# Performance work log

Measured on AMD Instinct MI355X. Metric: run time of the kernel, lower is better.

## Reference

```python
import jax, jax.numpy as jnp
import numpy as np

NEG_INF = -1e20

def setup_inputs() -> dict:
    key = jax.random.key(0)
    kq, kk, kv, km = jax.random.split(key, 4)
    B, S, H, D = 2, 2048, 16, 64
    queries = jax.random.normal(kq, (B, S, H, D), dtype=jnp.float32)
    keys = jax.random.normal(kk, (B, S, H, D), dtype=jnp.float32)
    values = jax.random.normal(kv, (B, S, H, D), dtype=jnp.float32)
    mask = jax.random.randint(km, (B, 1, 1, S), 0, 2, dtype=jnp.int32)
    return {"queries": queries, "keys": keys, "values": values, "mask": mask}

def reference(queries, keys, values, mask):
    # scores: [B, H, Q, K]
    dk = keys.shape[-1]
    scores = jnp.einsum('bqhd,bkhd->bhqk', queries, keys) / jnp.sqrt(jnp.asarray(dk, queries.dtype))
    scores = jnp.where(mask == 0, jnp.asarray(NEG_INF, scores.dtype), scores)
    attn = jax.nn.softmax(scores, axis=-1)
    # dropout p=0.0 (eval): identity
    out = jnp.einsum('bhqv,bvhd->bqhd', attn, values)
    return out
```

## Files before the change

### kernel.cpp

```cpp
#include <hip/hip_runtime.h>
#include <hip/hip_bf16.h>

#define S_LEN 2048
#define NH 16
#define HD 64

typedef __attribute__((ext_vector_type(8))) __bf16 bf16x8;
typedef __attribute__((ext_vector_type(16))) float f32x16;

#define QSCALE 0.1803368801111204f

static __device__ __forceinline__ ushort f2bf(float f) {
    unsigned int u = __float_as_uint(f);
    u += 0x7fffu + ((u >> 16) & 1u);
    return (ushort)(u >> 16);
}

static __device__ __forceinline__ void gload16(const void* g, void* l) {
    __builtin_amdgcn_global_load_lds(
        (const __attribute__((address_space(1))) unsigned int*)g,
        (__attribute__((address_space(3))) unsigned int*)l, 16, 0, 0);
}
static __device__ __forceinline__ void gload4(const void* g, void* l) {
    __builtin_amdgcn_global_load_lds(
        (const __attribute__((address_space(1))) unsigned int*)g,
        (__attribute__((address_space(3))) unsigned int*)l, 4, 0, 0);
}

static __device__ __forceinline__ unsigned cvtpk_bf16(float lo, float hi) {
    unsigned r;
    asm("v_cvt_pk_bf16_f32 %0, %1, %2" : "=v"(r) : "v"(lo), "v"(hi));
    return r;
}
static __device__ __forceinline__ float exp2_fast(float x) {
    float r;
    asm("v_exp_f32 %0, %1" : "=v"(r) : "v"(x));
    return r;
}

__global__ __launch_bounds__(256) void prep_k_kernel(const float* __restrict__ in,
                                                     ushort* __restrict__ out) {
    unsigned t = blockIdx.x * 256u + threadIdx.x;
    unsigned o = t & 7u;
    unsigned s = (t >> 3) & 2047u;
    unsigned bh = t >> 14;
    unsigned b = bh >> 4, h = bh & 15u;
    const float* src = in + (((size_t)(b * S_LEN) + s) * NH + h) * HD + o * 8;
    float4 x = *(const float4*)src;
    float4 y = *(const float4*)(src + 4);
    union { ushort u[8]; uint4 q; } fu;
    fu.u[0] = f2bf(x.x); fu.u[1] = f2bf(x.y); fu.u[2] = f2bf(x.z); fu.u[3] = f2bf(x.w);
    fu.u[4] = f2bf(y.x); fu.u[5] = f2bf(y.y); fu.u[6] = f2bf(y.z); fu.u[7] = f2bf(y.w);
    unsigned kt = s >> 6, kh = (s >> 5) & 1u, kl = s & 31u;
    unsigned dchunk = o >> 1, ho = o & 1u;
    size_t ci = (((size_t)(bh * 32u + kt) * 2u + kh) * 4u + dchunk) * 64u + kl + 32u * ho;
    *(uint4*)(out + ci * 8u) = fu.q;
}

__global__ __launch_bounds__(256) void prep_v_kernel(const float* __restrict__ in,
                                                     ushort* __restrict__ out) {
    __shared__ float T[64][68];
    const unsigned tid = threadIdx.x;
    const unsigned kt = blockIdx.x, bh = blockIdx.y;
    const unsigned b = bh >> 4, h = bh & 15u;
#pragma unroll
    for (int i = 0; i < 4; ++i) {
        unsigned idx = tid + i * 256u;
        unsigned sl = idx >> 4, d4 = (idx & 15u) * 4u;
        float4 v = *(const float4*)(in + (((size_t)(b * S_LEN) + kt * 64u + sl) * NH + h) * HD + d4);
        *(float4*)&T[sl][d4] = v;
    }
    __syncthreads();
#pragma unroll
    for (int it = 0; it < 2; ++it) {
        unsigned ct = tid + it * 256u;
        unsigned l = ct & 63u, sub = ct >> 6;
        unsigned nt = sub & 1u, c = (sub >> 1) & 1u, kh = sub >> 2;
        unsigned d = (l & 31u) + 32u * nt;
        unsigned kb = kh * 32u + c * 16u + (l >> 5) * 8u;
        union { ushort u[8]; uint4 q; } fu;
#pragma unroll
        for (int j = 0; j < 8; ++j) fu.u[j] = f2bf(T[kb + j][d]);
        *(uint4*)(out + ((size_t)(bh * 32u + kt) * 8u + sub) * 512u + l * 8u) = fu.q;
    }
}

struct TileMem {
    ushort K[2][3][2048];
    ushort V[2][3][2048];
    int    mk[2][1024];
};
struct CombMem {
    float ob[4][32][64];
    float lsb[4][64];
    float rls[4][32];
};
union SMemU { TileMem s; CombMem c; };

__global__ __launch_bounds__(512, 4) void attn_kernel(const float* __restrict__ Qp,
                                                      const ushort* __restrict__ Kws,
                                                      const ushort* __restrict__ Vws,
                                                      const int* __restrict__ maskp,
                                                      float* __restrict__ outp) {
    __shared__ __align__(16) SMemU sm;

    const unsigned tid = threadIdx.x;
    const unsigned wid = tid >> 6;
    const unsigned lane = tid & 63u;
    const unsigned l31 = lane & 31u;
    const unsigned hi = lane >> 5;
    const unsigned qsub = wid & 3u;
    const unsigned kgrp = wid >> 2;

    const unsigned bh = blockIdx.y;
    const unsigned b = bh >> 4, h = bh & 15u;
    const unsigned q0 = blockIdx.x * 128u + qsub * 32u;

    bf16x8 qf[4];
    {
        const float* qb = Qp + (((size_t)(b * S_LEN) + q0 + l31) * NH + h) * HD + hi * 8u;
#pragma unroll
        for (int dc = 0; dc < 4; ++dc) {
            float4 x = *(const float4*)(qb + dc * 16);
            float4 y = *(const float4*)(qb + dc * 16 + 4);
            union { ushort u[8]; bf16x8 v; } fu;
            fu.u[0] = f2bf(x.x * QSCALE); fu.u[1] = f2bf(x.y * QSCALE);
            fu.u[2] = f2bf(x.z * QSCALE); fu.u[3] = f2bf(x.w * QSCALE);
            fu.u[4] = f2bf(y.x * QSCALE); fu.u[5] = f2bf(y.y * QSCALE);
            fu.u[6] = f2bf(y.z * QSCALE); fu.u[7] = f2bf(y.w * QSCALE);
            qf[dc] = fu.v;
        }
    }

    f32x16 oacc0 = {0,0,0,0,0,0,0,0,0,0,0,0,0,0,0,0};
    f32x16 oacc1 = {0,0,0,0,0,0,0,0,0,0,0,0,0,0,0,0};
    float ls0 = 0.f, ls1 = 0.f, ls2 = 0.f, ls3 = 0.f;

    const char* kgp = (const char*)(Kws + (size_t)bh * 131072u
                    + (size_t)kgrp * 65536u) + qsub * 1024u + lane * 16u;
    const char* vgp = (const char*)(Vws + (size_t)bh * 131072u
                    + (size_t)kgrp * 65536u) + qsub * 1024u + lane * 16u;

    ushort* klb = &sm.s.K[kgrp][0][qsub * 512u];
    ushort* vlb = &sm.s.V[kgrp][0][qsub * 512u];
    const ushort* krd = &sm.s.K[kgrp][0][0];
    const ushort* vrd = &sm.s.V[kgrp][0][0];

#define STAGE(T, BUF) do {                                                     \
    const size_t toff = (size_t)(T) * 4096u;                                   \
    gload16(kgp + toff, klb + (BUF) * 2048u);                                  \
    gload16(vgp + toff, vlb + (BUF) * 2048u);                                  \
  } while (0)

    {
        const int* mgp = maskp + (size_t)b * S_LEN + kgrp * 1024u + qsub * 256u + lane;
#pragma unroll
        for (int j = 0; j < 4; ++j)
            gload4(mgp + j * 64, &sm.s.mk[kgrp][qsub * 256u + j * 64u]);
    }
    STAGE(0, 0u);
    STAGE(1, 1u);
    asm volatile("s_waitcnt vmcnt(2)" ::: "memory");
    __builtin_amdgcn_s_barrier();

    unsigned cur = 0u, st = 2u;
    for (int t = 0; t < 32; ++t) {
        if (t < 30) STAGE(t + 2, st);
        const ushort* kr = krd + cur * 2048u;
        const ushort* vr = vrd + cur * 2048u;
        const int*    mr = &sm.s.mk[kgrp][(unsigned)t * 32u];

        bf16x8 kf[4];
#pragma unroll
        for (int dc = 0; dc < 4; ++dc)
            kf[dc] = *(const bf16x8*)&kr[dc * 512u + lane * 8u];

        f32x16 s = {0,0,0,0,0,0,0,0,0,0,0,0,0,0,0,0};
        __builtin_amdgcn_s_setprio(1);
#pragma unroll
        for (int dc = 0; dc < 4; ++dc)
            s = __builtin_amdgcn_mfma_f32_32x32x16_bf16(kf[dc], qf[dc], s, 0, 0, 0);
        __builtin_amdgcn_s_setprio(0);

        float p[16];
#pragma unroll
        for (int r1 = 0; r1 < 4; ++r1) {
            int mv[4];
            *(int4*)mv = *(const int4*)&mr[r1 * 8 + hi * 4];
#pragma unroll
            for (int r0 = 0; r0 < 4; ++r0) {
                const int reg = r1 * 4 + r0;
                p[reg] = exp2_fast(mv[r0] ? s[reg] : -1e30f);
            }
            ls0 += p[r1 * 4 + 0]; ls1 += p[r1 * 4 + 1];
            ls2 += p[r1 * 4 + 2]; ls3 += p[r1 * 4 + 3];
        }

#pragma unroll
        for (int c = 0; c < 2; ++c) {
            unsigned a0 = cvtpk_bf16(p[8 * c + 0], p[8 * c + 1]);
            unsigned a1 = cvtpk_bf16(p[8 * c + 2], p[8 * c + 3]);
            unsigned b0 = cvtpk_bf16(p[8 * c + 4], p[8 * c + 5]);
            unsigned b1 = cvtpk_bf16(p[8 * c + 6], p[8 * c + 7]);
            asm("v_permlane32_swap_b32 %0, %1" : "+v"(a0), "+v"(b0));
            asm("v_permlane32_swap_b32 %0, %1" : "+v"(a1), "+v"(b1));
            union { unsigned w[4]; bf16x8 v; } pa;
            pa.w[0] = a0; pa.w[1] = a1; pa.w[2] = b0; pa.w[3] = b1;
            bf16x8 vf0 = *(const bf16x8*)&vr[(c * 2 + 0) * 512u + lane * 8u];
            bf16x8 vf1 = *(const bf16x8*)&vr[(c * 2 + 1) * 512u + lane * 8u];
            __builtin_amdgcn_s_setprio(1);
            oacc0 = __builtin_amdgcn_mfma_f32_32x32x16_bf16(pa.v, vf0, oacc0, 0, 0, 0);
            oacc1 = __builtin_amdgcn_mfma_f32_32x32x16_bf16(pa.v, vf1, oacc1, 0, 0, 0);
            __builtin_amdgcn_s_setprio(0);
        }

        if (t < 30) asm volatile("s_waitcnt vmcnt(2)" ::: "memory");
        else        asm volatile("s_waitcnt vmcnt(0)" ::: "memory");
        __builtin_amdgcn_s_barrier();
        cur = (cur == 2u) ? 0u : cur + 1u;
        st  = (st  == 2u) ? 0u : st  + 1u;
    }
#undef STAGE

    float lsum = (ls0 + ls1) + (ls2 + ls3);
    lsum += __shfl_xor(lsum, 32);

    if (kgrp == 1) {
#pragma unroll
        for (int r = 0; r < 16; ++r) {
            sm.c.ob[qsub][r][lane]      = oacc0[r];
            sm.c.ob[qsub][16 + r][lane] = oacc1[r];
        }
        sm.c.lsb[qsub][lane] = lsum;
    }
    __syncthreads();
    if (kgrp == 0) {
        lsum += sm.c.lsb[qsub][lane];
#pragma unroll
        for (int r = 0; r < 16; ++r) {
            oacc0[r] += sm.c.ob[qsub][r][lane];
            oacc1[r] += sm.c.ob[qsub][16 + r][lane];
        }
        if (hi == 0) sm.c.rls[qsub][l31] = 1.0f / lsum;
#pragma unroll
        for (int r1 = 0; r1 < 4; ++r1) {
#pragma unroll
            for (int r0 = 0; r0 < 4; ++r0) {
                const int reg = r1 * 4 + r0;
                const unsigned q = r0 + 8u * r1 + 4u * hi;
                const float rr = sm.c.rls[qsub][q];
                float* ob = outp + (((size_t)(b * S_LEN) + q0 + q) * NH + h) * HD + l31;
                ob[0]  = oacc0[reg] * rr;
                ob[32] = oacc1[reg] * rr;
            }
        }
    }
}

extern "C" void kernel_launch(void* const* d_in, const int* in_sizes, int n_in,
                              void* d_out, int out_size, void* d_ws, size_t ws_size,
                              hipStream_t stream) {
    const float* Qp = (const float*)d_in[0];
    const float* Kp = (const float*)d_in[1];
    const float* Vp = (const float*)d_in[2];
    const int* maskp = (const int*)d_in[3];
    float* outp = (float*)d_out;

    ushort* Kws = (ushort*)d_ws;
    ushort* Vws = Kws + (size_t)2 * NH * S_LEN * HD;

    hipLaunchKernelGGL(prep_k_kernel, dim3(2048), dim3(256), 0, stream, Kp, Kws);
    hipLaunchKernelGGL(prep_v_kernel, dim3(32, 32), dim3(256), 0, stream, Vp, Vws);
    hipLaunchKernelGGL(attn_kernel, dim3(S_LEN / 128, 32), dim3(512), 0, stream,
                       Qp, Kws, Vws, maskp, outp);
}
```

Measured before the change: 65.21 us.

## Software-pipeline QK^T of next tile with PV of current tile, 4-stage buffers

Restructures the main loop so the QK^T MFMA for tile j+1 is issued before the PV MFMA for tile j, with the softmax exp for j+1 computed afterwards. A prologue computes the first score tile. K/V LDS buffering grows from 3 to 4 stages with one more tile prefetched ahead. The intent is to overlap the exp/mask VALU work with matrix-core work and hide more load latency, at the cost of more LDS per block (which may reduce occupancy at 4 blocks/CU) and more live registers.

```diff
diff --git a/kernel.cpp b/kernel.cpp
--- a/kernel.cpp
+++ b/kernel.cpp
@@ -86,8 +86,8 @@
 }
 
 struct TileMem {
-    ushort K[2][3][2048];
-    ushort V[2][3][2048];
+    ushort K[2][4][2048];
+    ushort V[2][4][2048];
     int    mk[2][1024];
 };
 struct CombMem {
@@ -160,29 +160,23 @@
     }
     STAGE(0, 0u);
     STAGE(1, 1u);
+    STAGE(2, 2u);
     asm volatile("s_waitcnt vmcnt(2)" ::: "memory");
     __builtin_amdgcn_s_barrier();
 
-    unsigned cur = 0u, st = 2u;
-    for (int t = 0; t < 32; ++t) {
-        if (t < 30) STAGE(t + 2, st);
-        const ushort* kr = krd + cur * 2048u;
-        const ushort* vr = vrd + cur * 2048u;
-        const int*    mr = &sm.s.mk[kgrp][(unsigned)t * 32u];
-
+    float p[16];
+    {
         bf16x8 kf[4];
 #pragma unroll
         for (int dc = 0; dc < 4; ++dc)
-            kf[dc] = *(const bf16x8*)&kr[dc * 512u + lane * 8u];
-
+            kf[dc] = *(const bf16x8*)&krd[dc * 512u + lane * 8u];
         f32x16 s = {0,0,0,0,0,0,0,0,0,0,0,0,0,0,0,0};
         __builtin_amdgcn_s_setprio(1);
 #pragma unroll
         for (int dc = 0; dc < 4; ++dc)
             s = __builtin_amdgcn_mfma_f32_32x32x16_bf16(kf[dc], qf[dc], s, 0, 0, 0);
         __builtin_amdgcn_s_setprio(0);
-
-        float p[16];
+        const int* mr = &sm.s.mk[kgrp][0];
 #pragma unroll
         for (int r1 = 0; r1 < 4; ++r1) {
             int mv[4];
@@ -195,30 +189,67 @@
             ls0 += p[r1 * 4 + 0]; ls1 += p[r1 * 4 + 1];
             ls2 += p[r1 * 4 + 2]; ls3 += p[r1 * 4 + 3];
         }
-
-#pragma unroll
-        for (int c = 0; c < 2; ++c) {
-            unsigned a0 = cvtpk_bf16(p[8 * c + 0], p[8 * c + 1]);
-            unsigned a1 = cvtpk_bf16(p[8 * c + 2], p[8 * c + 3]);
-            unsigned b0 = cvtpk_bf16(p[8 * c + 4], p[8 * c + 5]);
-            unsigned b1 = cvtpk_bf16(p[8 * c + 6], p[8 * c + 7]);
-            asm("v_permlane32_swap_b32 %0, %1" : "+v"(a0), "+v"(b0));
-            asm("v_permlane32_swap_b32 %0, %1" : "+v"(a1), "+v"(b1));
-            union { unsigned w[4]; bf16x8 v; } pa;
-            pa.w[0] = a0; pa.w[1] = a1; pa.w[2] = b0; pa.w[3] = b1;
-            bf16x8 vf0 = *(const bf16x8*)&vr[(c * 2 + 0) * 512u + lane * 8u];
-            bf16x8 vf1 = *(const bf16x8*)&vr[(c * 2 + 1) * 512u + lane * 8u];
+    }
+
+    for (int j = 0; j < 32; ++j) {
+        if (j < 29) STAGE(j + 3, (unsigned)(j + 3) & 3u);
+
+        f32x16 s;
+        if (j < 31) {
+            const ushort* kr = krd + ((unsigned)(j + 1) & 3u) * 2048u;
+            bf16x8 kf[4];
+#pragma unroll
+            for (int dc = 0; dc < 4; ++dc)
+                kf[dc] = *(const bf16x8*)&kr[dc * 512u + lane * 8u];
+            f32x16 sz = {0,0,0,0,0,0,0,0,0,0,0,0,0,0,0,0};
             __builtin_amdgcn_s_setprio(1);
-            oacc0 = __builtin_amdgcn_mfma_f32_32x32x16_bf16(pa.v, vf0, oacc0, 0, 0, 0);
-            oacc1 = __builtin_amdgcn_mfma_f32_32x32x16_bf16(pa.v, vf1, oacc1, 0, 0, 0);
+#pragma unroll
+            for (int dc = 0; dc < 4; ++dc)
+                sz = __builtin_amdgcn_mfma_f32_32x32x16_bf16(kf[dc], qf[dc], sz, 0, 0, 0);
             __builtin_amdgcn_s_setprio(0);
-        }
-
-        if (t < 30) asm volatile("s_waitcnt vmcnt(2)" ::: "memory");
+            s = sz;
+        }
+
+        {
+            const ushort* vr = vrd + ((unsigned)j & 3u) * 2048u;
+#pragma unroll
+            for (int c = 0; c < 2; ++c) {
+                unsigned a0 = cvtpk_bf16(p[8 * c + 0], p[8 * c + 1]);
+                unsigned a1 = cvtpk_bf16(p[8 * c + 2], p[8 * c + 3]);
+                unsigned b0 = cvtpk_bf16(p[8 * c + 4], p[8 * c + 5]);
+                unsigned b1 = cvtpk_bf16(p[8 * c + 6], p[8 * c + 7]);
+                asm("v_permlane32_swap_b32 %0, %1" : "+v"(a0), "+v"(b0));
+                asm("v_permlane32_swap_b32 %0, %1" : "+v"(a1), "+v"(b1));
+                union { unsigned w[4]; bf16x8 v; } pa;
+                pa.w[0] = a0; pa.w[1] = a1; pa.w[2] = b0; pa.w[3] = b1;
+                bf16x8 vf0 = *(const bf16x8*)&vr[(c * 2 + 0) * 512u + lane * 8u];
+                bf16x8 vf1 = *(const bf16x8*)&vr[(c * 2 + 1) * 512u + lane * 8u];
+                __builtin_amdgcn_s_setprio(1);
+                oacc0 = __builtin_amdgcn_mfma_f32_32x32x16_bf16(pa.v, vf0, oacc0, 0, 0, 0);
+                oacc1 = __builtin_amdgcn_mfma_f32_32x32x16_bf16(pa.v, vf1, oacc1, 0, 0, 0);
+                __builtin_amdgcn_s_setprio(0);
+            }
+        }
+
+        if (j < 31) {
+            const int* mr = &sm.s.mk[kgrp][(unsigned)(j + 1) * 32u];
+#pragma unroll
+            for (int r1 = 0; r1 < 4; ++r1) {
+                int mv[4];
+                *(int4*)mv = *(const int4*)&mr[r1 * 8 + hi * 4];
+#pragma unroll
+                for (int r0 = 0; r0 < 4; ++r0) {
+                    const int reg = r1 * 4 + r0;
+                    p[reg] = exp2_fast(mv[r0] ? s[reg] : -1e30f);
+                }
+                ls0 += p[r1 * 4 + 0]; ls1 += p[r1 * 4 + 1];
+                ls2 += p[r1 * 4 + 2]; ls3 += p[r1 * 4 + 3];
+            }
+        }
+
+        if (j < 29) asm volatile("s_waitcnt vmcnt(2)" ::: "memory");
         else        asm volatile("s_waitcnt vmcnt(0)" ::: "memory");
         __builtin_amdgcn_s_barrier();
-        cur = (cur == 2u) ? 0u : cur + 1u;
-        st  = (st  == 2u) ? 0u : st  + 1u;
     }
 #undef STAGE
 
```

New measurement: 64.86 us. About the same (-0.5%).
